# Kernel optimization log

Measured on AMD Instinct MI355X. Metric: run time of the kernel, lower is better.

Reference implementation:

```python
import jax, jax.numpy as jnp
import numpy as np

B, C, H, W = 8, 512, 128, 128
WS = 8

def _proj(x, w, b):
    # 1x1 conv == channel GEMM: (B,C,H,W) x (Cout,Cin) -> (B,Cout,H,W)
    return jnp.einsum('bchw,oc->bohw', x, w) + b[None, :, None, None]

def _split_windows(x):
    # (B,C,H,W) -> (B*nH*nW, ws*ws, C)
    b, c, h, w = x.shape
    x = x.reshape(b, c, h // WS, WS, w // WS, WS)
    x = x.transpose(0, 2, 4, 3, 5, 1)
    return x.reshape(-1, WS * WS, c)

def _merge_windows(x, b, c, h, w):
    # (B*nH*nW, ws*ws, C) -> (B,C,H,W)
    x = x.reshape(b, h // WS, w // WS, WS, WS, c)
    x = x.transpose(0, 5, 1, 3, 2, 4)
    return x.reshape(b, c, h, w)

def setup_inputs() -> dict:
    key = jax.random.key(0)
    ks = jax.random.split(key, 9)
    s = 1.0 / np.sqrt(C)
    return {
        'x': jax.random.normal(ks[0], (B, C, H, W), jnp.float32),
        'wq': jax.random.normal(ks[1], (C, C), jnp.float32) * s,
        'bq': jnp.zeros((C,), jnp.float32),
        'wk': jax.random.normal(ks[2], (C, C), jnp.float32) * s,
        'bk': jnp.zeros((C,), jnp.float32),
        'wv': jax.random.normal(ks[3], (C, C), jnp.float32) * s,
        'bv': jnp.zeros((C,), jnp.float32),
        'wo': jax.random.normal(ks[4], (C, C), jnp.float32) * s,
        'bo': jnp.zeros((C,), jnp.float32),
    }

def reference(x, wq, bq, wk, bk, wv, bv, wo, bo):
    b, c, h, w = x.shape
    q = _split_windows(_proj(x, wq, bq))  # (nWin, ws*ws, C)
    k = _split_windows(_proj(x, wk, bk))
    v = _split_windows(_proj(x, wv, bv))
    attn = jnp.einsum('nqc,nkc->nqk', q, k) / jnp.sqrt(jnp.asarray(c, x.dtype))
    attn = jax.nn.softmax(attn, axis=-1)
    out = jnp.einsum('nqk,nkc->nqc', attn, v)
    out = _merge_windows(out, b, c, h, w)
    return _proj(out, wo, bo)
```

## Files before the change

kernel.cpp:

```cpp
#include <hip/hip_runtime.h>

typedef __attribute__((ext_vector_type(8))) short bf16x8;
typedef __attribute__((ext_vector_type(4))) float f32x4;

#define MFMA16(a, b, c) __builtin_amdgcn_mfma_f32_16x16x32_bf16((a), (b), (c), 0, 0, 0)

__device__ __forceinline__ float b2f(unsigned short u) {
  unsigned int v = ((unsigned int)u) << 16;
  return __builtin_bit_cast(float, v);
}
__device__ __forceinline__ unsigned short f2b(float f) {
  unsigned int u = __builtin_bit_cast(unsigned int, f);
  u += 0x7fffu + ((u >> 16) & 1u);
  return (unsigned short)(u >> 16);
}
__device__ __forceinline__ void gload16(const void* g, void* l) {
  __builtin_amdgcn_global_load_lds(
      (const __attribute__((address_space(1))) unsigned int*)g,
      (__attribute__((address_space(3))) unsigned int*)l, 16, 0, 0);
}

__global__ __launch_bounds__(256) void k_wconv(
    const float* __restrict__ src, unsigned short* __restrict__ dst) {
  const int i = (blockIdx.x * 256 + threadIdx.x) * 4;
  const float4 v = *(const float4*)(src + i);
  uint2 p;
  p.x = (unsigned int)f2b(v.x) | ((unsigned int)f2b(v.y) << 16);
  p.y = (unsigned int)f2b(v.z) | ((unsigned int)f2b(v.w) << 16);
  *(uint2*)(dst + i) = p;
}

__global__ __launch_bounds__(256) void k_wtrans(
    const float* __restrict__ in, unsigned short* __restrict__ out) {
  __shared__ unsigned short tile[64][72];
  const int r0 = blockIdx.x << 6, s0 = blockIdx.y << 6;
  const int t = threadIdx.x;
  {
    const int sl = t >> 3, rl = (t & 7) << 3;
#pragma unroll
    for (int pass = 0; pass < 2; ++pass) {
      const int s = sl + pass * 32;
      const float* src = in + (size_t)(s0 + s) * 512 + r0 + rl;
      const float4 f0 = ((const float4*)src)[0];
      const float4 f1 = ((const float4*)src)[1];
      tile[rl + 0][s] = f2b(f0.x);
      tile[rl + 1][s] = f2b(f0.y);
      tile[rl + 2][s] = f2b(f0.z);
      tile[rl + 3][s] = f2b(f0.w);
      tile[rl + 4][s] = f2b(f1.x);
      tile[rl + 5][s] = f2b(f1.y);
      tile[rl + 6][s] = f2b(f1.z);
      tile[rl + 7][s] = f2b(f1.w);
    }
  }
  __syncthreads();
  {
    const int rl = t >> 3, sl = (t & 7) << 3;
#pragma unroll
    for (int pass = 0; pass < 2; ++pass) {
      const int r = rl + pass * 32;
      uint4 v = *(const uint4*)&tile[r][sl];
      *(uint4*)(out + (size_t)(r0 + r) * 512 + s0 + sl) = v;
    }
  }
}

__global__ __launch_bounds__(256) void k_bvo(
    const float* __restrict__ wo, const float* __restrict__ bv,
    const float* __restrict__ bo, float* __restrict__ bvo) {
  const int o = blockIdx.x * 256 + threadIdx.x;
  float acc = bo[o];
  const float* row = wo + (size_t)o * 512;
  for (int j = 0; j < 512; ++j) acc += row[j] * bv[j];
  bvo[o] = acc;
}

__global__ __launch_bounds__(256) void k_ub(
    const float* __restrict__ wk, const float* __restrict__ bq,
    float* __restrict__ u) {
  const int c = blockIdx.x * 256 + threadIdx.x;
  float acc = 0.f;
  for (int o = 0; o < 512; ++o) acc += bq[o] * wk[(size_t)o * 512 + c];
  u[c] = acc;
}

__global__ __launch_bounds__(256) void k_transpose(
    const float* __restrict__ X, unsigned short* __restrict__ XT,
    unsigned short* __restrict__ XV) {
  __shared__ unsigned short tile[32][528];
  const int bx = blockIdx.x;
  const int wt = bx & 1, ht = bx >> 1;
  const int c0 = blockIdx.y << 5;
  const int b = blockIdx.z;
  const int w0 = wt << 6, h0 = ht << 3;
  const int t = threadIdx.x;
  const int cl = t >> 3, wl = t & 7;

  const float* xsrc = X + (size_t)b * 8388608u + (size_t)(c0 + cl) * 16384 +
                      (size_t)h0 * 128 + w0 + wl * 8;
  const int winb = b * 256 + ht * 16 + wt * 8;
  unsigned short* xvdst =
      XV + (size_t)(c0 + cl) * 131072 + (size_t)(winb + wl) * 64;

#pragma unroll
  for (int hh = 0; hh < 8; ++hh) {
    const float4 f0 = ((const float4*)(xsrc + hh * 128))[0];
    const float4 f1 = ((const float4*)(xsrc + hh * 128))[1];
    unsigned short r8[8];
    r8[0] = f2b(f0.x); r8[1] = f2b(f0.y); r8[2] = f2b(f0.z); r8[3] = f2b(f0.w);
    r8[4] = f2b(f1.x); r8[5] = f2b(f1.y); r8[6] = f2b(f1.z); r8[7] = f2b(f1.w);
    *(uint4*)&tile[cl][hh * 64 + wl * 8] = *(const uint4*)r8;
    *(uint4*)(xvdst + hh * 8) = *(const uint4*)r8;
  }
  __syncthreads();

  unsigned short* xtb = XT + (size_t)b * 8388608u;
#pragma unroll
  for (int pp = 0; pp < 2; ++pp) {
    const int pl = t + pp * 256;
    const int hh = pl >> 6, ww = pl & 63;
    unsigned short buf[32];
#pragma unroll
    for (int c = 0; c < 32; ++c) buf[c] = tile[c][pl];
    unsigned short* dst =
        xtb + ((size_t)(h0 + hh) * 128 + w0 + ww) * 512 + c0;
    *(uint4*)(dst + 0) = *(const uint4*)&buf[0];
    *(uint4*)(dst + 8) = *(const uint4*)&buf[8];
    *(uint4*)(dst + 16) = *(const uint4*)&buf[16];
    *(uint4*)(dst + 24) = *(const uint4*)&buf[24];
  }
}

template <int MODE>
__global__ __launch_bounds__(512, 2) void k_gemm256(
    const unsigned short* __restrict__ A, const unsigned short* __restrict__ B,
    const float* __restrict__ bias0, void* __restrict__ C0v) {
  __shared__ unsigned short lsA[4][256 * 32];
  __shared__ unsigned short lsB[4][256 * 32];
  const int bid = blockIdx.x;
  int mt, nt;
  if (MODE == 0) {
    const int work = ((bid & 7) << 7) + (bid >> 3);
    mt = work >> 1; nt = work & 1;
  } else if (MODE == 2) {
    const int work = ((bid & 7) << 7) + (bid >> 3);
    nt = work >> 1; mt = work & 1;
  } else {
    mt = bid & 1; nt = bid >> 1;
  }
  const int m0 = mt << 8, n0 = nt << 8;

  const int t = threadIdx.x;
  const int l = t & 63;
  const int lr = l & 15, lg = l >> 4;
  const int w = t >> 6;
  const int wr = w >> 2, wc = w & 3;
  const int ra = wr << 7, rb = wc << 6;
  const int srowS = t >> 2;
  const int scolS = (t & 3) << 3;

  f32x4 acc[8][4];
#pragma unroll
  for (int i = 0; i < 8; ++i)
#pragma unroll
    for (int j = 0; j < 4; ++j) acc[i][j] = f32x4{0.f, 0.f, 0.f, 0.f};

  auto stage = [&](int kt) {
    const int buf = kt & 3, k0 = kt << 5;
#pragma unroll
    for (int hh = 0; hh < 2; ++hh) {
      gload16(A + (size_t)(m0 + srowS + hh * 128) * 512 + k0 + scolS,
              &lsA[buf][(srowS + hh * 128) * 32 + scolS]);
      gload16(B + (size_t)(n0 + srowS + hh * 128) * 512 + k0 + scolS,
              &lsB[buf][(srowS + hh * 128) * 32 + scolS]);
    }
  };
  auto compute = [&](int kt) {
    const int buf = kt & 3;
    bf16x8 af[8], bfv[4];
#pragma unroll
    for (int i = 0; i < 8; ++i)
      af[i] = *(const bf16x8*)&lsA[buf][(ra + i * 16 + lr) * 32 + lg * 8];
#pragma unroll
    for (int j = 0; j < 4; ++j)
      bfv[j] = *(const bf16x8*)&lsB[buf][(rb + j * 16 + lr) * 32 + lg * 8];
    __builtin_amdgcn_s_setprio(1);
#pragma unroll
    for (int i = 0; i < 8; ++i)
#pragma unroll
      for (int j = 0; j < 4; ++j)
        acc[i][j] = MFMA16(af[i], bfv[j], acc[i][j]);
    __builtin_amdgcn_s_setprio(0);
  };

  stage(0); stage(1); stage(2);

#define GITER(kt, vm)                                        \
  asm volatile("s_waitcnt vmcnt(" #vm ")" ::: "memory");     \
  __builtin_amdgcn_s_barrier();                              \
  __builtin_amdgcn_sched_barrier(0);                         \
  if ((kt) + 3 < 16) stage((kt) + 3);                        \
  compute(kt);                                               \
  __builtin_amdgcn_sched_barrier(0);                         \
  __builtin_amdgcn_s_barrier();

  GITER(0, 8)  GITER(1, 8)  GITER(2, 8)  GITER(3, 8)
  GITER(4, 8)  GITER(5, 8)  GITER(6, 8)  GITER(7, 8)
  GITER(8, 8)  GITER(9, 8)  GITER(10, 8) GITER(11, 8)
  GITER(12, 8) GITER(13, 8) GITER(14, 4) GITER(15, 0)
#undef GITER

#pragma unroll
  for (int i = 0; i < 8; ++i) {
    const int cmb = m0 + ra + i * 16 + lg * 4;
#pragma unroll
    for (int j = 0; j < 4; ++j) {
      const int cn = n0 + rb + j * 16 + lr;
      const float bn = (MODE == 0) ? bias0[cn] : 0.f;
#pragma unroll
      for (int r = 0; r < 4; ++r) {
        const int cm = cmb + r;
        if (MODE == 0) {
          ((unsigned short*)C0v)[(size_t)cm * 512 + cn] = f2b(acc[i][j][r] + bn);
        } else if (MODE == 2) {
          const float val = acc[i][j][r] + bias0[cm];
          const int bb = cn >> 14, p = cn & 16383;
          ((float*)C0v)[(size_t)bb * 8388608 + (size_t)cm * 16384 + p] = val;
        } else {
          ((unsigned short*)C0v)[(size_t)cm * 512 + cn] = f2b(acc[i][j][r]);
        }
      }
    }
  }
}

__global__ __launch_bounds__(256) void k_attn(
    const unsigned short* __restrict__ Q, const unsigned short* __restrict__ XT,
    const unsigned short* __restrict__ XV, unsigned short* __restrict__ Y) {
  __shared__ unsigned short P_lds[64][72];
  const int win = ((blockIdx.x & 7) << 8) + (blockIdx.x >> 3);
  const int b = win >> 8, th = (win >> 4) & 15, tw = win & 15;
  const size_t p_base = (size_t)b * 16384 + (size_t)th * 1024 + (size_t)tw * 8;
  const int t = threadIdx.x, w = t >> 6, l = t & 63;
  const int lr = l & 15, lg = l >> 4;
  const int qs = w << 4;
  const int qtok = qs + lr;
  const unsigned short* qrow =
      Q + (p_base + (size_t)(qtok >> 3) * 128 + (qtok & 7)) * 512;
  const unsigned short* krow =
      XT + (p_base + (size_t)(lr >> 3) * 128 + (lr & 7)) * 512;

  f32x4 acc[4];
#pragma unroll
  for (int i = 0; i < 4; ++i) acc[i] = f32x4{0.f, 0.f, 0.f, 0.f};

  bf16x8 bqp[2], akp[2][4];
#pragma unroll
  for (int pp = 0; pp < 2; ++pp) {
    const int co = pp * 32 + lg * 8;
    bqp[pp] = *(const bf16x8*)(qrow + co);
#pragma unroll
    for (int mt = 0; mt < 4; ++mt)
      akp[pp][mt] = *(const bf16x8*)(krow + (size_t)mt * 131072 + co);
  }
#pragma unroll
  for (int cs = 0; cs < 16; ++cs) {
    const int cb = cs & 1;
    bf16x8 bqn;
    bf16x8 akn[4];
    if (cs + 2 < 16) {
      const int co = (cs + 2) * 32 + lg * 8;
      bqn = *(const bf16x8*)(qrow + co);
#pragma unroll
      for (int mt = 0; mt < 4; ++mt)
        akn[mt] = *(const bf16x8*)(krow + (size_t)mt * 131072 + co);
    }
    __builtin_amdgcn_s_setprio(1);
#pragma unroll
    for (int mt = 0; mt < 4; ++mt)
      acc[mt] = MFMA16(akp[cb][mt], bqp[cb], acc[mt]);
    __builtin_amdgcn_s_setprio(0);
    if (cs + 2 < 16) {
      bqp[cb] = bqn;
#pragma unroll
      for (int mt = 0; mt < 4; ++mt) akp[cb][mt] = akn[mt];
    }
  }

  const float scale = 0.044194173824159216f;
  float pv[4][4];
  float mx = -3.0e38f;
#pragma unroll
  for (int mt = 0; mt < 4; ++mt)
#pragma unroll
    for (int j = 0; j < 4; ++j) {
      const float s = acc[mt][j] * scale;
      pv[mt][j] = s;
      mx = fmaxf(mx, s);
    }
  mx = fmaxf(mx, __shfl_xor(mx, 16));
  mx = fmaxf(mx, __shfl_xor(mx, 32));
  float sum = 0.f;
#pragma unroll
  for (int mt = 0; mt < 4; ++mt)
#pragma unroll
    for (int j = 0; j < 4; ++j) {
      const float e = __expf(pv[mt][j] - mx);
      pv[mt][j] = e;
      sum += e;
    }
  sum += __shfl_xor(sum, 16);
  sum += __shfl_xor(sum, 32);
  const float inv = 1.f / sum;

#pragma unroll
  for (int mt = 0; mt < 4; ++mt)
#pragma unroll
    for (int j = 0; j < 4; j += 2) {
      const unsigned int pk =
          (unsigned int)f2b(pv[mt][j] * inv) |
          ((unsigned int)f2b(pv[mt][j + 1] * inv) << 16);
      *(unsigned int*)&P_lds[qtok][mt * 16 + lg * 4 + j] = pk;
    }
  __syncthreads();

  const bf16x8 pa0 = *(const bf16x8*)&P_lds[qtok][lg * 8];
  const bf16x8 pa1 = *(const bf16x8*)&P_lds[qtok][32 + lg * 8];
  const unsigned short* vbase =
      XV + (size_t)lr * 131072 + (size_t)win * 64 + lg * 8;
  unsigned short* ybase[4];
#pragma unroll
  for (int r = 0; r < 4; ++r) {
    const int qq = qs + lg * 4 + r;
    ybase[r] =
        Y + (p_base + (size_t)(qq >> 3) * 128 + (qq & 7)) * 512 + lr;
  }
  bf16x8 v0p[2], v1p[2];
#pragma unroll
  for (int pp = 0; pp < 2; ++pp) {
    const unsigned short* vp = vbase + (size_t)pp * (16 * 131072);
    v0p[pp] = *(const bf16x8*)vp;
    v1p[pp] = *(const bf16x8*)(vp + 32);
  }
#pragma unroll
  for (int nt = 0; nt < 32; ++nt) {
    const int cb = nt & 1;
    bf16x8 v0n, v1n;
    if (nt + 2 < 32) {
      const unsigned short* vp = vbase + (size_t)(nt + 2) * (16 * 131072);
      v0n = *(const bf16x8*)vp;
      v1n = *(const bf16x8*)(vp + 32);
    }
    f32x4 o = f32x4{0.f, 0.f, 0.f, 0.f};
    __builtin_amdgcn_s_setprio(1);
    o = MFMA16(pa0, v0p[cb], o);
    o = MFMA16(pa1, v1p[cb], o);
    __builtin_amdgcn_s_setprio(0);
#pragma unroll
    for (int r = 0; r < 4; ++r) ybase[r][nt * 16] = f2b(o[r]);
    if (nt + 2 < 32) {
      v0p[cb] = v0n;
      v1p[cb] = v1n;
    }
  }
}

extern "C" void kernel_launch(void* const* d_in, const int* in_sizes, int n_in,
                              void* d_out, int out_size, void* d_ws,
                              size_t ws_size, hipStream_t stream) {
  (void)in_sizes; (void)n_in; (void)out_size;
  const float* x = (const float*)d_in[0];
  const float* wq = (const float*)d_in[1];
  const float* bq = (const float*)d_in[2];
  const float* wk = (const float*)d_in[3];
  const float* bk = (const float*)d_in[4];
  const float* wv = (const float*)d_in[5];
  const float* bv = (const float*)d_in[6];
  const float* wo = (const float*)d_in[7];
  const float* bo = (const float*)d_in[8];
  (void)bk;

  const size_t NEED = (size_t)(2097152 + 3 * 67108864) * 2;
  if (ws_size < NEED) return;

  unsigned short* wb = (unsigned short*)d_ws;
  unsigned short* wqT = wb;
  unsigned short* wkT = wb + 262144;
  unsigned short* wvT = wb + 524288;
  unsigned short* wo_b = wb + 786432;
  unsigned short* wvo = wb + 1048576;
  float* bvo = (float*)(wb + 1310720);
  float* ub = (float*)(wb + 1311744);
  unsigned short* Bqk = wb + 1572864;
  unsigned short* xT = wb + 2097152;
  unsigned short* xV = xT + 67108864;
  unsigned short* Ybuf = xV + 67108864;
  unsigned short* Tq = (unsigned short*)d_out;

  k_wtrans<<<dim3(8, 8), 256, 0, stream>>>(wq, wqT);
  k_wtrans<<<dim3(8, 8), 256, 0, stream>>>(wk, wkT);
  k_wtrans<<<dim3(8, 8), 256, 0, stream>>>(wv, wvT);
  k_wconv<<<256, 256, 0, stream>>>(wo, wo_b);
  k_gemm256<3><<<4, 512, 0, stream>>>(wkT, wqT, nullptr, Bqk);
  k_gemm256<3><<<4, 512, 0, stream>>>(wo_b, wvT, nullptr, wvo);
  k_ub<<<2, 256, 0, stream>>>(wk, bq, ub);
  k_bvo<<<2, 256, 0, stream>>>(wo, bv, bo, bvo);
  k_transpose<<<dim3(32, 16, 8), 256, 0, stream>>>(x, xT, xV);
  k_gemm256<0><<<1024, 512, 0, stream>>>(xT, Bqk, ub, Tq);
  k_attn<<<2048, 256, 0, stream>>>(Tq, xT, xV, Ybuf);
  k_gemm256<2><<<1024, 512, 0, stream>>>(wvo, Ybuf, bvo, d_out);
}
```

Before: 637.7 us.

## Assign one full window per wavefront in attention kernel

The attention kernel now gives each of the four wavefronts a whole 64-token window, where before four wavefronts shared one window by splitting its query rows. Each wave computes all 16 QK^T tiles and all 4 PV query tiles itself, and the grid shrinks from 2048 to 512 blocks. The goal is to load each K and V fragment once per window instead of once per wave, and to drop the block-wide __syncthreads, since each wave now has its own P buffer in LDS. In exchange, register pressure rises (a 4x4 accumulator array plus four Q fragments), which may lower occupancy, and there are fewer blocks to spread across the CUs.

```diff
diff --git a/kernel.cpp b/kernel.cpp
--- a/kernel.cpp
+++ b/kernel.cpp
@@ -237,104 +237,102 @@
 __global__ __launch_bounds__(256) void k_attn(
     const unsigned short* __restrict__ Q, const unsigned short* __restrict__ XT,
     const unsigned short* __restrict__ XV, unsigned short* __restrict__ Y) {
-  __shared__ unsigned short P_lds[64][72];
-  const int win = ((blockIdx.x & 7) << 8) + (blockIdx.x >> 3);
+  __shared__ unsigned short P_lds[4][64][72];
+  const int t = threadIdx.x, w = t >> 6, l = t & 63;
+  const int lr = l & 15, lg = l >> 4;
+  const int grp = ((blockIdx.x & 7) << 6) + (blockIdx.x >> 3);
+  const int win = grp * 4 + w;
   const int b = win >> 8, th = (win >> 4) & 15, tw = win & 15;
   const size_t p_base = (size_t)b * 16384 + (size_t)th * 1024 + (size_t)tw * 8;
-  const int t = threadIdx.x, w = t >> 6, l = t & 63;
-  const int lr = l & 15, lg = l >> 4;
-  const int qs = w << 4;
-  const int qtok = qs + lr;
-  const unsigned short* qrow =
-      Q + (p_base + (size_t)(qtok >> 3) * 128 + (qtok & 7)) * 512;
-  const unsigned short* krow =
-      XT + (p_base + (size_t)(lr >> 3) * 128 + (lr & 7)) * 512;
-
-  f32x4 acc[4];
-#pragma unroll
-  for (int i = 0; i < 4; ++i) acc[i] = f32x4{0.f, 0.f, 0.f, 0.f};
-
-  bf16x8 bqp[2], akp[2][4];
+  const size_t rowpix = p_base + (size_t)(lr >> 3) * 128 + (lr & 7);
+  const unsigned short* qbase = Q + rowpix * 512;
+  const unsigned short* kbase = XT + rowpix * 512;
+
+  f32x4 acc[4][4];
+#pragma unroll
+  for (int i = 0; i < 4; ++i)
+#pragma unroll
+    for (int j = 0; j < 4; ++j) acc[i][j] = f32x4{0.f, 0.f, 0.f, 0.f};
+
+  bf16x8 kp[2][4], qp[2][4];
 #pragma unroll
   for (int pp = 0; pp < 2; ++pp) {
     const int co = pp * 32 + lg * 8;
-    bqp[pp] = *(const bf16x8*)(qrow + co);
-#pragma unroll
-    for (int mt = 0; mt < 4; ++mt)
-      akp[pp][mt] = *(const bf16x8*)(krow + (size_t)mt * 131072 + co);
+#pragma unroll
+    for (int i = 0; i < 4; ++i) {
+      kp[pp][i] = *(const bf16x8*)(kbase + (size_t)i * 131072 + co);
+      qp[pp][i] = *(const bf16x8*)(qbase + (size_t)i * 131072 + co);
+    }
   }
 #pragma unroll
   for (int cs = 0; cs < 16; ++cs) {
     const int cb = cs & 1;
-    bf16x8 bqn;
-    bf16x8 akn[4];
+    __builtin_amdgcn_s_setprio(1);
+#pragma unroll
+    for (int mt = 0; mt < 4; ++mt)
+#pragma unroll
+      for (int qt = 0; qt < 4; ++qt)
+        acc[mt][qt] = MFMA16(kp[cb][mt], qp[cb][qt], acc[mt][qt]);
+    __builtin_amdgcn_s_setprio(0);
     if (cs + 2 < 16) {
       const int co = (cs + 2) * 32 + lg * 8;
-      bqn = *(const bf16x8*)(qrow + co);
-#pragma unroll
-      for (int mt = 0; mt < 4; ++mt)
-        akn[mt] = *(const bf16x8*)(krow + (size_t)mt * 131072 + co);
-    }
-    __builtin_amdgcn_s_setprio(1);
+#pragma unroll
+      for (int i = 0; i < 4; ++i) {
+        kp[cb][i] = *(const bf16x8*)(kbase + (size_t)i * 131072 + co);
+        qp[cb][i] = *(const bf16x8*)(qbase + (size_t)i * 131072 + co);
+      }
+    }
+  }
+
+  const float scale = 0.044194173824159216f;
+#pragma unroll
+  for (int qt = 0; qt < 4; ++qt) {
+    float pv[4][4];
+    float mx = -3.0e38f;
 #pragma unroll
     for (int mt = 0; mt < 4; ++mt)
-      acc[mt] = MFMA16(akp[cb][mt], bqp[cb], acc[mt]);
-    __builtin_amdgcn_s_setprio(0);
-    if (cs + 2 < 16) {
-      bqp[cb] = bqn;
-#pragma unroll
-      for (int mt = 0; mt < 4; ++mt) akp[cb][mt] = akn[mt];
-    }
-  }
-
-  const float scale = 0.044194173824159216f;
-  float pv[4][4];
-  float mx = -3.0e38f;
-#pragma unroll
-  for (int mt = 0; mt < 4; ++mt)
-#pragma unroll
-    for (int j = 0; j < 4; ++j) {
-      const float s = acc[mt][j] * scale;
-      pv[mt][j] = s;
-      mx = fmaxf(mx, s);
-    }
-  mx = fmaxf(mx, __shfl_xor(mx, 16));
-  mx = fmaxf(mx, __shfl_xor(mx, 32));
-  float sum = 0.f;
-#pragma unroll
-  for (int mt = 0; mt < 4; ++mt)
-#pragma unroll
-    for (int j = 0; j < 4; ++j) {
-      const float e = __expf(pv[mt][j] - mx);
-      pv[mt][j] = e;
-      sum += e;
-    }
-  sum += __shfl_xor(sum, 16);
-  sum += __shfl_xor(sum, 32);
-  const float inv = 1.f / sum;
-
-#pragma unroll
-  for (int mt = 0; mt < 4; ++mt)
-#pragma unroll
-    for (int j = 0; j < 4; j += 2) {
-      const unsigned int pk =
-          (unsigned int)f2b(pv[mt][j] * inv) |
-          ((unsigned int)f2b(pv[mt][j + 1] * inv) << 16);
-      *(unsigned int*)&P_lds[qtok][mt * 16 + lg * 4 + j] = pk;
-    }
-  __syncthreads();
-
-  const bf16x8 pa0 = *(const bf16x8*)&P_lds[qtok][lg * 8];
-  const bf16x8 pa1 = *(const bf16x8*)&P_lds[qtok][32 + lg * 8];
+#pragma unroll
+      for (int j = 0; j < 4; ++j) {
+        const float s = acc[mt][qt][j] * scale;
+        pv[mt][j] = s;
+        mx = fmaxf(mx, s);
+      }
+    mx = fmaxf(mx, __shfl_xor(mx, 16));
+    mx = fmaxf(mx, __shfl_xor(mx, 32));
+    float sum = 0.f;
+#pragma unroll
+    for (int mt = 0; mt < 4; ++mt)
+#pragma unroll
+      for (int j = 0; j < 4; ++j) {
+        const float e = __expf(pv[mt][j] - mx);
+        pv[mt][j] = e;
+        sum += e;
+      }
+    sum += __shfl_xor(sum, 16);
+    sum += __shfl_xor(sum, 32);
+    const float inv = 1.f / sum;
+#pragma unroll
+    for (int mt = 0; mt < 4; ++mt)
+#pragma unroll
+      for (int j = 0; j < 4; j += 2) {
+        const unsigned int pk =
+            (unsigned int)f2b(pv[mt][j] * inv) |
+            ((unsigned int)f2b(pv[mt][j + 1] * inv) << 16);
+        *(unsigned int*)&P_lds[w][qt * 16 + lr][mt * 16 + lg * 4 + j] = pk;
+      }
+  }
+
+  bf16x8 pa0[4], pa1[4];
+#pragma unroll
+  for (int qt = 0; qt < 4; ++qt) {
+    pa0[qt] = *(const bf16x8*)&P_lds[w][qt * 16 + lr][lg * 8];
+    pa1[qt] = *(const bf16x8*)&P_lds[w][qt * 16 + lr][32 + lg * 8];
+  }
   const unsigned short* vbase =
       XV + (size_t)lr * 131072 + (size_t)win * 64 + lg * 8;
-  unsigned short* ybase[4];
-#pragma unroll
-  for (int r = 0; r < 4; ++r) {
-    const int qq = qs + lg * 4 + r;
-    ybase[r] =
-        Y + (p_base + (size_t)(qq >> 3) * 128 + (qq & 7)) * 512 + lr;
-  }
+  unsigned short* ystore =
+      Y + (p_base + (size_t)(lg >> 1) * 128 + ((lg & 1) << 2)) * 512 + lr;
+
   bf16x8 v0p[2], v1p[2];
 #pragma unroll
   for (int pp = 0; pp < 2; ++pp) {
@@ -345,23 +343,25 @@
 #pragma unroll
   for (int nt = 0; nt < 32; ++nt) {
     const int cb = nt & 1;
-    bf16x8 v0n, v1n;
+    f32x4 o[4];
+    __builtin_amdgcn_s_setprio(1);
+#pragma unroll
+    for (int qt = 0; qt < 4; ++qt) {
+      o[qt] = f32x4{0.f, 0.f, 0.f, 0.f};
+      o[qt] = MFMA16(pa0[qt], v0p[cb], o[qt]);
+      o[qt] = MFMA16(pa1[qt], v1p[cb], o[qt]);
+    }
+    __builtin_amdgcn_s_setprio(0);
     if (nt + 2 < 32) {
       const unsigned short* vp = vbase + (size_t)(nt + 2) * (16 * 131072);
-      v0n = *(const bf16x8*)vp;
-      v1n = *(const bf16x8*)(vp + 32);
-    }
-    f32x4 o = f32x4{0.f, 0.f, 0.f, 0.f};
-    __builtin_amdgcn_s_setprio(1);
-    o = MFMA16(pa0, v0p[cb], o);
-    o = MFMA16(pa1, v1p[cb], o);
-    __builtin_amdgcn_s_setprio(0);
-#pragma unroll
-    for (int r = 0; r < 4; ++r) ybase[r][nt * 16] = f2b(o[r]);
-    if (nt + 2 < 32) {
-      v0p[cb] = v0n;
-      v1p[cb] = v1n;
-    }
+      v0p[cb] = *(const bf16x8*)vp;
+      v1p[cb] = *(const bf16x8*)(vp + 32);
+    }
+#pragma unroll
+    for (int qt = 0; qt < 4; ++qt)
+#pragma unroll
+      for (int r = 0; r < 4; ++r)
+        ystore[(size_t)qt * 131072 + r * 512 + nt * 16] = f2b(o[qt][r]);
   }
 }
 
@@ -407,6 +407,6 @@
   k_bvo<<<2, 256, 0, stream>>>(wo, bv, bo, bvo);
   k_transpose<<<dim3(32, 16, 8), 256, 0, stream>>>(x, xT, xV);
   k_gemm256<0><<<1024, 512, 0, stream>>>(xT, Bqk, ub, Tq);
-  k_attn<<<2048, 256, 0, stream>>>(Tq, xT, xV, Ybuf);
+  k_attn<<<512, 256, 0, stream>>>(Tq, xT, xV, Ybuf);
   k_gemm256<2><<<1024, 512, 0, stream>>>(wvo, Ybuf, bvo, d_out);
 }
```

Result: faster. 587.9 us (-7.8%).
